# Optimization experiments

Measured on AMD Instinct MI355X. Metric: run time of the kernel, lower is better.

## Reference

```python
import jax, jax.numpy as jnp
import numpy as np


def _conv1x1(x, w, b):
    # x: (B, C, H, W), w: (O, C), b: (O,)  -> (B, O, H, W)
    return jnp.einsum('oc,bchw->bohw', w, x) + b[None, :, None, None]


def _branch(xq, xkv, wq, bq, wk, bk, wv, bv):
    B, C, H, W = xq.shape
    N = H * W
    q = _conv1x1(xq, wq, bq).reshape(B, -1, N)   # (B, d, N)
    k = _conv1x1(xkv, wk, bk).reshape(B, -1, N)  # (B, d, N)
    v = _conv1x1(xkv, wv, bv).reshape(B, C, N)   # (B, C, N)
    energy = jnp.einsum('bdi,bdj->bij', q, k)    # (B, N, N), no scale (as in source)
    attn = jax.nn.softmax(energy, axis=-1)
    out = jnp.einsum('bcj,bij->bci', v, attn)    # bmm(v, attn^T)
    return out.reshape(B, C, H, W)


def setup_inputs() -> dict:
    key = jax.random.key(0)
    ks = jax.random.split(key, 16)
    B, C, H, W = 4, 256, 64, 64
    d = C // 8
    s_in = 0.02
    inp = {
        'x1': jax.random.normal(ks[0], (B, C, H, W), jnp.float32),
        'x2': jax.random.normal(ks[1], (B, C, H, W), jnp.float32),
        'wq1': jax.random.normal(ks[2], (d, C), jnp.float32) * s_in,
        'bq1': jnp.zeros((d,), jnp.float32),
        'wk1': jax.random.normal(ks[3], (d, C), jnp.float32) * s_in,
        'bk1': jnp.zeros((d,), jnp.float32),
        'wv1': jax.random.normal(ks[4], (C, C), jnp.float32) * s_in,
        'bv1': jnp.zeros((C,), jnp.float32),
        'wq2': jax.random.normal(ks[5], (d, C), jnp.float32) * s_in,
        'bq2': jnp.zeros((d,), jnp.float32),
        'wk2': jax.random.normal(ks[6], (d, C), jnp.float32) * s_in,
        'bk2': jnp.zeros((d,), jnp.float32),
        'wv2': jax.random.normal(ks[7], (C, C), jnp.float32) * s_in,
        'bv2': jnp.zeros((C,), jnp.float32),
    }
    return inp


def reference(x1, x2, wq1, bq1, wk1, bk1, wv1, bv1, wq2, bq2, wk2, bk2, wv2, bv2):
    out1 = _branch(x1, x2, wq1, bq1, wk1, bk1, wv1, bv1)
    out2 = _branch(x1, x2, wq2, bq2, wk2, bk2, wv2, bv2)
    return x1 + x2 + out1 + out2
```

## Files before the change

kernel.cpp:

```cpp
#include <hip/hip_runtime.h>

#define N_TOK 4096
#define C_DIM 256
#define D_DIM 32

typedef float f32x4 __attribute__((ext_vector_type(4)));
typedef short short8 __attribute__((ext_vector_type(8)));
typedef unsigned short u16;

__device__ __forceinline__ u16 f2bf(float f) {
    unsigned int u = __builtin_bit_cast(unsigned int, f);
    u += 0x7fffu + ((u >> 16) & 1u);
    return (u16)(u >> 16);
}
__device__ __forceinline__ u16 f2bf_fast(float f) {
    return (u16)((__builtin_bit_cast(unsigned int, f) + 0x8000u) >> 16);
}
__device__ __forceinline__ float bf2f(u16 h) {
    unsigned int u = ((unsigned int)h) << 16;
    return __builtin_bit_cast(float, u);
}
__device__ __forceinline__ float exp2_fast(float x) {
#if __has_builtin(__builtin_amdgcn_exp2f)
    return __builtin_amdgcn_exp2f(x);
#else
    return exp2f(x);
#endif
}


__global__ __launch_bounds__(256) void qk_proj(
    const float* __restrict__ x1, const float* __restrict__ x2,
    const float* __restrict__ wq1, const float* __restrict__ bq1,
    const float* __restrict__ wk1, const float* __restrict__ bk1,
    const float* __restrict__ wq2, const float* __restrict__ bq2,
    const float* __restrict__ wk2, const float* __restrict__ bk2,
    u16* __restrict__ wsQ, u16* __restrict__ wsK)
{
    __shared__ float w_lds[32 * 256];
    const int ib = blockIdx.x;
    const int comb = blockIdx.y;
    const int b = comb & 3;
    const int branch = (comb >> 2) & 1;
    const int qk = comb >> 3;

    const float* x = qk ? x2 : x1;
    const float* w; const float* bias; u16* dst;
    if (qk == 0) { w = branch ? wq2 : wq1; bias = branch ? bq2 : bq1; dst = wsQ; }
    else         { w = branch ? wk2 : wk1; bias = branch ? bk2 : bk1; dst = wsK; }
    const int slice = branch * 4 + b;
    dst += (size_t)slice * N_TOK * D_DIM;
    const float osc = (qk == 0) ? 1.44269504088896341f : 1.0f;

    const int tid = threadIdx.x;
    for (int t = tid; t < 32 * 256; t += 256) w_lds[t] = w[t];
    __syncthreads();

    const int il = tid & 63;
    const int db = tid >> 6;
    const float* xc = x + (size_t)b * C_DIM * N_TOK + ib * 64 + il;

    float acc[8] = {0.f,0.f,0.f,0.f,0.f,0.f,0.f,0.f};
    for (int c4 = 0; c4 < 256; c4 += 4) {
        const float xv0 = xc[(size_t)(c4 + 0) * N_TOK];
        const float xv1 = xc[(size_t)(c4 + 1) * N_TOK];
        const float xv2 = xc[(size_t)(c4 + 2) * N_TOK];
        const float xv3 = xc[(size_t)(c4 + 3) * N_TOK];
#pragma unroll
        for (int mm = 0; mm < 8; ++mm) {
            const float4 wv = *(const float4*)&w_lds[(db * 8 + mm) * 256 + c4];
            acc[mm] += xv0 * wv.x + xv1 * wv.y + xv2 * wv.z + xv3 * wv.w;
        }
    }
    short8 pack;
#pragma unroll
    for (int mm = 0; mm < 8; ++mm)
        pack[mm] = (short)f2bf((acc[mm] + bias[db * 8 + mm]) * osc);
    *(short8*)(dst + (size_t)(ib * 64 + il) * D_DIM + db * 8) = pack;
}

__device__ __forceinline__ void stage_xt(u16* xtb, const float* xb, int ks,
                                         int wave, int lane)
{
    const int j  = (wave & 1) * 64 + lane;
    const int cb = (wave >> 1) * 16;
    const float* xp = xb + (size_t)(ks * 32 + cb) * N_TOK + j;
    u16 vals[16];
#pragma unroll
    for (int qq = 0; qq < 16; ++qq) vals[qq] = f2bf(xp[(size_t)qq * N_TOK]);
    const int swz = (j >> 1) & 3;
    u16* row = xtb + j * 32;
    const int c0 = cb >> 3;
    *(short8*)&row[((c0    ) ^ swz) * 8] = *(const short8*)&vals[0];
    *(short8*)&row[((c0 + 1) ^ swz) * 8] = *(const short8*)&vals[8];
}

__global__ __launch_bounds__(256, 2) void v_proj(
    const float* __restrict__ x2,
    const float* __restrict__ wv1, const float* __restrict__ bv1,
    const float* __restrict__ wv2, const float* __restrict__ bv2,
    u16* __restrict__ wsV)
{
    __shared__ __align__(16) u16 wl[128 * 256];
    __shared__ __align__(16) u16 xt[2][128 * 32];

    const int jt = blockIdx.x, ct = blockIdx.y, s = blockIdx.z;
    const int branch = s >> 2, b = s & 3;
    const float* w    = branch ? wv2 : wv1;
    const float* bias = branch ? bv2 : bv1;
    u16* dst = wsV + (size_t)s * C_DIM * N_TOK;
    const float* xb = x2 + (size_t)b * C_DIM * N_TOK + jt * 128;

    const int tid = threadIdx.x;
    const int wave = tid >> 6, lane = tid & 63;
    const int wr = wave >> 1, wc = wave & 1;
    const int g = lane >> 4, li = lane & 15;

    {
        const int c = tid >> 1;
        const int kh = (tid & 1) * 128;
        const float* wrow = w + (size_t)(ct * 128 + c) * C_DIM + kh;
        u16* lrow = wl + c * 256;
#pragma unroll
        for (int kk = 0; kk < 128; kk += 8) {
            const float4 a0 = *(const float4*)&wrow[kk];
            const float4 a1 = *(const float4*)&wrow[kk + 4];
            u16 tmp[8] = {f2bf(a0.x), f2bf(a0.y), f2bf(a0.z), f2bf(a0.w),
                          f2bf(a1.x), f2bf(a1.y), f2bf(a1.z), f2bf(a1.w)};
            const int kc = (kh + kk) >> 3;
            *(short8*)&lrow[(kc ^ (c & 7)) * 8] = *(const short8*)tmp;
        }
    }
    stage_xt(&xt[0][0], xb, 0, wave, lane);
    __syncthreads();

    f32x4 acc[4][4];
#pragma unroll
    for (int mf = 0; mf < 4; ++mf)
#pragma unroll
        for (int nf = 0; nf < 4; ++nf) acc[mf][nf] = (f32x4){0.f, 0.f, 0.f, 0.f};

    int buf = 0;
    for (int ks = 0; ks < 8; ++ks) {
        if (ks < 7) stage_xt(&xt[buf ^ 1][0], xb, ks + 1, wave, lane);

        short8 af[4], bf[4];
#pragma unroll
        for (int mf = 0; mf < 4; ++mf) {
            const int c = wr * 64 + mf * 16 + li;
            af[mf] = *(const short8*)&wl[c * 256 + (((ks * 4 + g) ^ (li & 7)) * 8)];
        }
#pragma unroll
        for (int nf = 0; nf < 4; ++nf) {
            const int j = wc * 64 + nf * 16 + li;
            bf[nf] = *(const short8*)&xt[buf][j * 32 + ((g ^ ((j >> 1) & 3)) * 8)];
        }
        __builtin_amdgcn_s_setprio(1);
#pragma unroll
        for (int mf = 0; mf < 4; ++mf)
#pragma unroll
            for (int nf = 0; nf < 4; ++nf)
                acc[mf][nf] = __builtin_amdgcn_mfma_f32_16x16x32_bf16(
                    af[mf], bf[nf], acc[mf][nf], 0, 0, 0);
        __builtin_amdgcn_s_setprio(0);
        __syncthreads();
        buf ^= 1;
    }

#pragma unroll
    for (int mf = 0; mf < 4; ++mf) {
#pragma unroll
        for (int r = 0; r < 4; ++r) {
            const int c = ct * 128 + wr * 64 + mf * 16 + 4 * g + r;
            const float bv = bias[c];
            const int cswz = (c >> 1) & 3;
            u16* crow = dst + c * 32;
#pragma unroll
            for (int nf = 0; nf < 4; ++nf) {
                const int j = jt * 128 + wc * 64 + nf * 16 + li;
                const int pos = ((j >> 3) & 3) ^ cswz;
                crow[(size_t)(j >> 5) * 8192 + pos * 8 + (j & 7)] =
                    f2bf(acc[mf][nf][r] + bv);
            }
        }
    }
}

__global__ __launch_bounds__(256, 4) void attn_fwd(
    const u16* __restrict__ Q, const u16* __restrict__ K,
    const u16* __restrict__ V, u16* __restrict__ O)
{
    __shared__ __align__(16) short vlds[2][2][128 * 32];
    __shared__ float lscr[2][2][64][2];

    const int n  = blockIdx.x;
    const int s  = n & 7;
    const int ib = (n >> 3) & 63;
    const int ct = n >> 9;
    const u16* q = Q + (size_t)s * N_TOK * D_DIM;
    const u16* k = K + (size_t)s * N_TOK * D_DIM;
    const u16* v = V + (size_t)s * C_DIM * N_TOK + ct * 4096;
    u16*       o = O + (size_t)s * N_TOK * C_DIM + ct * 128;

    const int tid  = threadIdx.x;
    const int wave = tid >> 6;
    const int lane = tid & 63;
    const int grp  = wave >> 1;
    const int wg   = wave & 1;
    const int g    = lane >> 4;
    const int li   = lane & 15;
    const int i0   = ib * 64 + wg * 32;
    const int jbase = grp * (N_TOK / 2);
    const int NP = N_TOK / 2 / 32;

    short8 qf[2];
    qf[0] = *(const short8*)(q + (size_t)(i0 + li) * D_DIM + 8 * g);
    qf[1] = *(const short8*)(q + (size_t)(i0 + 16 + li) * D_DIM + 8 * g);

    f32x4 acc[2][8];
#pragma unroll
    for (int it = 0; it < 2; ++it)
#pragma unroll
        for (int cf = 0; cf < 8; ++cf) acc[it][cf] = (f32x4){0.f, 0.f, 0.f, 0.f};
    float lsum[2] = {0.f, 0.f};

    const int roff = (g ^ ((li >> 1) & 3)) << 3;

    {
        const u16* tile = v + (size_t)(jbase >> 5) * 8192;
#pragma unroll
        for (int ii = 0; ii < 4; ++ii) {
            const int off = (wg * 4 + ii) * 512;
            __builtin_amdgcn_global_load_lds(
                (const __attribute__((address_space(1))) void*)(tile + off + lane * 8),
                (__attribute__((address_space(3))) void*)(&vlds[grp][0][0] + off),
                16, 0, 0);
        }
    }
    __syncthreads();

    int buf = 0;
    for (int p = 0; p < NP; ++p) {
        if (p < NP - 1) {
            const u16* tile = v + (size_t)((jbase + (p + 1) * 32) >> 5) * 8192;
            short* dst = &vlds[grp][buf ^ 1][0];
#pragma unroll
            for (int ii = 0; ii < 4; ++ii) {
                const int off = (wg * 4 + ii) * 512;
                __builtin_amdgcn_global_load_lds(
                    (const __attribute__((address_space(1))) void*)(tile + off + lane * 8),
                    (__attribute__((address_space(3))) void*)(dst + off),
                    16, 0, 0);
            }
        }

        const int j0 = jbase + p * 32;
        const short8 ke = *(const short8*)(k + (size_t)(j0 + 2 * li    ) * D_DIM + 8 * g);
        const short8 ko = *(const short8*)(k + (size_t)(j0 + 2 * li + 1) * D_DIM + 8 * g);

        const f32x4 z = (f32x4){0.f, 0.f, 0.f, 0.f};
        short8 pa[2];
#pragma unroll
        for (int it = 0; it < 2; ++it) {
            f32x4 se = __builtin_amdgcn_mfma_f32_16x16x32_bf16(ke, qf[it], z, 0, 0, 0);
            f32x4 so = __builtin_amdgcn_mfma_f32_16x16x32_bf16(ko, qf[it], z, 0, 0, 0);
            float pe[4], po[4];
#pragma unroll
            for (int r = 0; r < 4; ++r) {
                pe[r] = exp2_fast(se[r]);
                po[r] = exp2_fast(so[r]);
            }
            lsum[it] += ((pe[0] + po[0]) + (pe[1] + po[1]))
                      + ((pe[2] + po[2]) + (pe[3] + po[3]));
#pragma unroll
            for (int r = 0; r < 4; ++r) {
                pa[it][2 * r]     = (short)f2bf_fast(pe[r]);
                pa[it][2 * r + 1] = (short)f2bf_fast(po[r]);
            }
        }

        const short* vb = &vlds[grp][buf][0];
        __builtin_amdgcn_s_setprio(1);
#pragma unroll
        for (int cf = 0; cf < 8; ++cf) {
            const short8 vf = *(const short8*)&vb[(cf * 16 + li) * 32 + roff];
            acc[0][cf] = __builtin_amdgcn_mfma_f32_16x16x32_bf16(pa[0], vf, acc[0][cf], 0, 0, 0);
            acc[1][cf] = __builtin_amdgcn_mfma_f32_16x16x32_bf16(pa[1], vf, acc[1][cf], 0, 0, 0);
        }
        __builtin_amdgcn_s_setprio(0);
        __syncthreads();
        buf ^= 1;
    }

#pragma unroll
    for (int it = 0; it < 2; ++it) {
        lsum[it] += __shfl_xor(lsum[it], 16);
        lsum[it] += __shfl_xor(lsum[it], 32);
        lscr[grp][wg][lane][it] = lsum[it];
    }

    f32x4* pv = (f32x4*)&vlds[0][0][0];
#pragma unroll
    for (int it = 0; it < 2; ++it) {
        __syncthreads();
        if (grp == 1) {
#pragma unroll
            for (int cf = 0; cf < 8; ++cf)
                pv[(wg * 8 + cf) * 64 + lane] = acc[it][cf];
        }
        __syncthreads();
        if (grp == 0) {
#pragma unroll
            for (int cf = 0; cf < 8; ++cf) {
                const f32x4 o4 = pv[(wg * 8 + cf) * 64 + lane];
                acc[it][cf][0] += o4[0]; acc[it][cf][1] += o4[1];
                acc[it][cf][2] += o4[2]; acc[it][cf][3] += o4[3];
            }
        }
    }

    if (grp == 0) {
#pragma unroll
        for (int it = 0; it < 2; ++it) {
            const float linv = 1.0f / (lscr[0][wg][lane][it] + lscr[1][wg][lane][it]);
            float lr[4];
#pragma unroll
            for (int r = 0; r < 4; ++r) lr[r] = __shfl(linv, 4 * g + r);
#pragma unroll
            for (int cf = 0; cf < 8; ++cf)
#pragma unroll
                for (int r = 0; r < 4; ++r)
                    o[(size_t)(i0 + it * 16 + 4 * g + r) * C_DIM + cf * 16 + li] =
                        f2bf(acc[it][cf][r] * lr[r]);
        }
    }
}

__global__ __launch_bounds__(256) void epilogue(
    const float* __restrict__ x1, const float* __restrict__ x2,
    const u16* __restrict__ O, float* __restrict__ out)
{
    __shared__ float tl[64][65];
    const int it = blockIdx.x, ct = blockIdx.y, b = blockIdx.z;
    const int tid = threadIdx.x;
    const int cl = tid & 63, r0 = tid >> 6;

    const u16* O1 = O + (size_t)(b)     * N_TOK * C_DIM;
    const u16* O2 = O + (size_t)(4 + b) * N_TOK * C_DIM;

#pragma unroll
    for (int rr = 0; rr < 16; ++rr) {
        const int il = r0 + rr * 4;
        const size_t off = (size_t)(it * 64 + il) * C_DIM + ct * 64 + cl;
        tl[il][cl] = bf2f(O1[off]) + bf2f(O2[off]);
    }
    __syncthreads();
#pragma unroll
    for (int rr = 0; rr < 16; ++rr) {
        const int c2 = r0 + rr * 4;
        const size_t idx = ((size_t)b * C_DIM + ct * 64 + c2) * N_TOK + it * 64 + cl;
        out[idx] = x1[idx] + x2[idx] + tl[cl][c2];
    }
}

extern "C" void kernel_launch(void* const* d_in, const int* in_sizes, int n_in,
                              void* d_out, int out_size, void* d_ws, size_t ws_size,
                              hipStream_t stream)
{
    const float* x1  = (const float*)d_in[0];
    const float* x2  = (const float*)d_in[1];
    const float* wq1 = (const float*)d_in[2];
    const float* bq1 = (const float*)d_in[3];
    const float* wk1 = (const float*)d_in[4];
    const float* bk1 = (const float*)d_in[5];
    const float* wv1 = (const float*)d_in[6];
    const float* bv1 = (const float*)d_in[7];
    const float* wq2 = (const float*)d_in[8];
    const float* bq2 = (const float*)d_in[9];
    const float* wk2 = (const float*)d_in[10];
    const float* bk2 = (const float*)d_in[11];
    const float* wv2 = (const float*)d_in[12];
    const float* bv2 = (const float*)d_in[13];
    float* out = (float*)d_out;

    u16* wsQ = (u16*)d_ws;
    u16* wsK = wsQ + (size_t)8 * N_TOK * D_DIM;
    u16* wsV = wsK + (size_t)8 * N_TOK * D_DIM;
    u16* wsO = wsV + (size_t)8 * C_DIM * N_TOK;

    qk_proj<<<dim3(64, 16), 256, 0, stream>>>(x1, x2, wq1, bq1, wk1, bk1,
                                              wq2, bq2, wk2, bk2, wsQ, wsK);
    v_proj<<<dim3(32, 2, 8), 256, 0, stream>>>(x2, wv1, bv1, wv2, bv2, wsV);
    attn_fwd<<<dim3(1024), 256, 0, stream>>>(wsQ, wsK, wsV, wsO);
    epilogue<<<dim3(64, 4, 4), 256, 0, stream>>>(x1, x2, wsO, out);
}
```

Before: 161.8 us.

## Triple-buffer V tiles and prefetch K two iterations ahead in attention loop

```diff
diff --git a/kernel.cpp b/kernel.cpp
--- a/kernel.cpp
+++ b/kernel.cpp
@@ -186,11 +186,24 @@
     }
 }
 
+__device__ __forceinline__ void stage_v32c(const u16* vhalf, short* dst,
+                                           int wg, int lane, int j0)
+{
+    const u16* tile = vhalf + (size_t)(j0 >> 5) * 8192;
+#pragma unroll
+    for (int ii = 0; ii < 4; ++ii) {
+        const int off = (wg * 4 + ii) * 512;
+        __builtin_amdgcn_global_load_lds(
+            (const __attribute__((address_space(1))) void*)(tile + off + lane * 8),
+            (__attribute__((address_space(3))) void*)(dst + off), 16, 0, 0);
+    }
+}
+
 __global__ __launch_bounds__(256, 4) void attn_fwd(
     const u16* __restrict__ Q, const u16* __restrict__ K,
     const u16* __restrict__ V, u16* __restrict__ O)
 {
-    __shared__ __align__(16) short vlds[2][2][128 * 32];
+    __shared__ __align__(16) short vlds[2][3][128 * 32];
     __shared__ float lscr[2][2][64][2];
 
     const int n  = blockIdx.x;
@@ -226,44 +239,30 @@
 
     const int roff = (g ^ ((li >> 1) & 3)) << 3;
 
-    {
-        const u16* tile = v + (size_t)(jbase >> 5) * 8192;
-#pragma unroll
-        for (int ii = 0; ii < 4; ++ii) {
-            const int off = (wg * 4 + ii) * 512;
-            __builtin_amdgcn_global_load_lds(
-                (const __attribute__((address_space(1))) void*)(tile + off + lane * 8),
-                (__attribute__((address_space(3))) void*)(&vlds[grp][0][0] + off),
-                16, 0, 0);
-        }
-    }
-    __syncthreads();
-
-    int buf = 0;
+    stage_v32c(v, &vlds[grp][0][0], wg, lane, jbase);
+    short8 keC = *(const short8*)(k + (size_t)(jbase + 2 * li    ) * D_DIM + 8 * g);
+    short8 koC = *(const short8*)(k + (size_t)(jbase + 2 * li + 1) * D_DIM + 8 * g);
+    stage_v32c(v, &vlds[grp][1][0], wg, lane, jbase + 32);
+    short8 keN = *(const short8*)(k + (size_t)(jbase + 32 + 2 * li) * D_DIM + 8 * g);
+    short8 koN = *(const short8*)(k + (size_t)(jbase + 33 + 2 * li) * D_DIM + 8 * g);
+    asm volatile("s_waitcnt vmcnt(8)" ::: "memory");
+    __builtin_amdgcn_s_barrier();
+
+    int bcur = 0;
     for (int p = 0; p < NP; ++p) {
-        if (p < NP - 1) {
-            const u16* tile = v + (size_t)((jbase + (p + 1) * 32) >> 5) * 8192;
-            short* dst = &vlds[grp][buf ^ 1][0];
-#pragma unroll
-            for (int ii = 0; ii < 4; ++ii) {
-                const int off = (wg * 4 + ii) * 512;
-                __builtin_amdgcn_global_load_lds(
-                    (const __attribute__((address_space(1))) void*)(tile + off + lane * 8),
-                    (__attribute__((address_space(3))) void*)(dst + off),
-                    16, 0, 0);
-            }
-        }
-
-        const int j0 = jbase + p * 32;
-        const short8 ke = *(const short8*)(k + (size_t)(j0 + 2 * li    ) * D_DIM + 8 * g);
-        const short8 ko = *(const short8*)(k + (size_t)(j0 + 2 * li + 1) * D_DIM + 8 * g);
+        int t2 = p + 2; if (t2 >= NP) t2 -= NP;
+        const int j2 = jbase + t2 * 32;
+        int b2 = bcur + 2; if (b2 >= 3) b2 -= 3;
+        stage_v32c(v, &vlds[grp][b2][0], wg, lane, j2);
+        const short8 ket = *(const short8*)(k + (size_t)(j2 + 2 * li    ) * D_DIM + 8 * g);
+        const short8 kot = *(const short8*)(k + (size_t)(j2 + 2 * li + 1) * D_DIM + 8 * g);
 
         const f32x4 z = (f32x4){0.f, 0.f, 0.f, 0.f};
         short8 pa[2];
 #pragma unroll
         for (int it = 0; it < 2; ++it) {
-            f32x4 se = __builtin_amdgcn_mfma_f32_16x16x32_bf16(ke, qf[it], z, 0, 0, 0);
-            f32x4 so = __builtin_amdgcn_mfma_f32_16x16x32_bf16(ko, qf[it], z, 0, 0, 0);
+            f32x4 se = __builtin_amdgcn_mfma_f32_16x16x32_bf16(keC, qf[it], z, 0, 0, 0);
+            f32x4 so = __builtin_amdgcn_mfma_f32_16x16x32_bf16(koC, qf[it], z, 0, 0, 0);
             float pe[4], po[4];
 #pragma unroll
             for (int r = 0; r < 4; ++r) {
@@ -279,7 +278,7 @@
             }
         }
 
-        const short* vb = &vlds[grp][buf][0];
+        const short* vb = &vlds[grp][bcur][0];
         __builtin_amdgcn_s_setprio(1);
 #pragma unroll
         for (int cf = 0; cf < 8; ++cf) {
@@ -288,8 +287,12 @@
             acc[1][cf] = __builtin_amdgcn_mfma_f32_16x16x32_bf16(pa[1], vf, acc[1][cf], 0, 0, 0);
         }
         __builtin_amdgcn_s_setprio(0);
-        __syncthreads();
-        buf ^= 1;
+
+        asm volatile("s_waitcnt vmcnt(8)" ::: "memory");
+        __builtin_amdgcn_s_barrier();
+
+        keC = keN; koC = koN; keN = ket; koN = kot;
+        bcur = (bcur == 2) ? 0 : bcur + 1;
     }
 
 #pragma unroll
```

Measured after the change: 215.5 us. 33.2% more time.

## Store V and softmax probabilities in FP8 and use FP8 MFMA for PV

Applied to the files above, without the earlier changes.

```diff
diff --git a/kernel.cpp b/kernel.cpp
--- a/kernel.cpp
+++ b/kernel.cpp
@@ -1,4 +1,5 @@
 #include <hip/hip_runtime.h>
+#include <hip/hip_fp8.h>
 
 #define N_TOK 4096
 #define C_DIM 256
@@ -7,14 +8,13 @@
 typedef float f32x4 __attribute__((ext_vector_type(4)));
 typedef short short8 __attribute__((ext_vector_type(8)));
 typedef unsigned short u16;
+typedef unsigned char u8;
+typedef long long i64;
 
 __device__ __forceinline__ u16 f2bf(float f) {
     unsigned int u = __builtin_bit_cast(unsigned int, f);
     u += 0x7fffu + ((u >> 16) & 1u);
     return (u16)(u >> 16);
-}
-__device__ __forceinline__ u16 f2bf_fast(float f) {
-    return (u16)((__builtin_bit_cast(unsigned int, f) + 0x8000u) >> 16);
 }
 __device__ __forceinline__ float bf2f(u16 h) {
     unsigned int u = ((unsigned int)h) << 16;
@@ -26,6 +26,19 @@
 #else
     return exp2f(x);
 #endif
+}
+template<bool HI>
+__device__ __forceinline__ int pk_fp8(float a, float b, int old) {
+#if __has_builtin(__builtin_amdgcn_cvt_pk_fp8_f32)
+    return __builtin_amdgcn_cvt_pk_fp8_f32(a, b, old, HI);
+#else
+    __hip_fp8_e4m3 fa(a), fb(b);
+    int v = (int)fa.__x | ((int)fb.__x << 8);
+    return HI ? ((old & 0xffff) | (v << 16)) : ((old & ~0xffff) | (v & 0xffff));
+#endif
+}
+__device__ __forceinline__ u8 f2fp8(float f) {
+    return (u8)(pk_fp8<false>(f, f, 0) & 0xff);
 }
 
 
@@ -99,7 +112,7 @@
     const float* __restrict__ x2,
     const float* __restrict__ wv1, const float* __restrict__ bv1,
     const float* __restrict__ wv2, const float* __restrict__ bv2,
-    u16* __restrict__ wsV)
+    u8* __restrict__ wsV)
 {
     __shared__ __align__(16) u16 wl[128 * 256];
     __shared__ __align__(16) u16 xt[2][128 * 32];
@@ -108,7 +121,7 @@
     const int branch = s >> 2, b = s & 3;
     const float* w    = branch ? wv2 : wv1;
     const float* bias = branch ? bv2 : bv1;
-    u16* dst = wsV + (size_t)s * C_DIM * N_TOK;
+    u8* dstB = wsV + (size_t)s * N_TOK * C_DIM;
     const float* xb = x2 + (size_t)b * C_DIM * N_TOK + jt * 128;
 
     const int tid = threadIdx.x;
@@ -173,14 +186,11 @@
         for (int r = 0; r < 4; ++r) {
             const int c = ct * 128 + wr * 64 + mf * 16 + 4 * g + r;
             const float bv = bias[c];
-            const int cswz = (c >> 1) & 3;
-            u16* crow = dst + c * 32;
 #pragma unroll
             for (int nf = 0; nf < 4; ++nf) {
                 const int j = jt * 128 + wc * 64 + nf * 16 + li;
-                const int pos = ((j >> 3) & 3) ^ cswz;
-                crow[(size_t)(j >> 5) * 8192 + pos * 8 + (j & 7)] =
-                    f2bf(acc[mf][nf][r] + bv);
+                dstB[(size_t)(j >> 5) * 8192 + ((j >> 3) & 3) * 2048
+                     + c * 8 + (j & 7)] = f2fp8(acc[mf][nf][r] + bv);
             }
         }
     }
@@ -188,9 +198,9 @@
 
 __global__ __launch_bounds__(256, 4) void attn_fwd(
     const u16* __restrict__ Q, const u16* __restrict__ K,
-    const u16* __restrict__ V, u16* __restrict__ O)
-{
-    __shared__ __align__(16) short vlds[2][2][128 * 32];
+    const u8* __restrict__ V, u16* __restrict__ O)
+{
+    __shared__ __align__(16) u8 vlds[2][2][4096];
     __shared__ float lscr[2][2][64][2];
 
     const int n  = blockIdx.x;
@@ -199,7 +209,7 @@
     const int ct = n >> 9;
     const u16* q = Q + (size_t)s * N_TOK * D_DIM;
     const u16* k = K + (size_t)s * N_TOK * D_DIM;
-    const u16* v = V + (size_t)s * C_DIM * N_TOK + ct * 4096;
+    const u8*  v = V + (size_t)s * N_TOK * C_DIM + ct * 1024;
     u16*       o = O + (size_t)s * N_TOK * C_DIM + ct * 128;
 
     const int tid  = threadIdx.x;
@@ -224,16 +234,14 @@
         for (int cf = 0; cf < 8; ++cf) acc[it][cf] = (f32x4){0.f, 0.f, 0.f, 0.f};
     float lsum[2] = {0.f, 0.f};
 
-    const int roff = (g ^ ((li >> 1) & 3)) << 3;
-
     {
-        const u16* tile = v + (size_t)(jbase >> 5) * 8192;
-#pragma unroll
-        for (int ii = 0; ii < 4; ++ii) {
-            const int off = (wg * 4 + ii) * 512;
+        const u8* tile = v + (size_t)(jbase >> 5) * 8192;
+#pragma unroll
+        for (int ii = 0; ii < 2; ++ii) {
+            const int p = wg * 2 + ii;
             __builtin_amdgcn_global_load_lds(
-                (const __attribute__((address_space(1))) void*)(tile + off + lane * 8),
-                (__attribute__((address_space(3))) void*)(&vlds[grp][0][0] + off),
+                (const __attribute__((address_space(1))) void*)(tile + p * 2048 + lane * 16),
+                (__attribute__((address_space(3))) void*)(&vlds[grp][0][0] + p * 1024),
                 16, 0, 0);
         }
     }
@@ -242,14 +250,14 @@
     int buf = 0;
     for (int p = 0; p < NP; ++p) {
         if (p < NP - 1) {
-            const u16* tile = v + (size_t)((jbase + (p + 1) * 32) >> 5) * 8192;
-            short* dst = &vlds[grp][buf ^ 1][0];
-#pragma unroll
-            for (int ii = 0; ii < 4; ++ii) {
-                const int off = (wg * 4 + ii) * 512;
+            const u8* tile = v + (size_t)((jbase + (p + 1) * 32) >> 5) * 8192;
+            u8* dst = &vlds[grp][buf ^ 1][0];
+#pragma unroll
+            for (int ii = 0; ii < 2; ++ii) {
+                const int pc = wg * 2 + ii;
                 __builtin_amdgcn_global_load_lds(
-                    (const __attribute__((address_space(1))) void*)(tile + off + lane * 8),
-                    (__attribute__((address_space(3))) void*)(dst + off),
+                    (const __attribute__((address_space(1))) void*)(tile + pc * 2048 + lane * 16),
+                    (__attribute__((address_space(3))) void*)(dst + pc * 1024),
                     16, 0, 0);
             }
         }
@@ -259,7 +267,7 @@
         const short8 ko = *(const short8*)(k + (size_t)(j0 + 2 * li + 1) * D_DIM + 8 * g);
 
         const f32x4 z = (f32x4){0.f, 0.f, 0.f, 0.f};
-        short8 pa[2];
+        i64 paL[2];
 #pragma unroll
         for (int it = 0; it < 2; ++it) {
             f32x4 se = __builtin_amdgcn_mfma_f32_16x16x32_bf16(ke, qf[it], z, 0, 0, 0);
@@ -272,20 +280,21 @@
             }
             lsum[it] += ((pe[0] + po[0]) + (pe[1] + po[1]))
                       + ((pe[2] + po[2]) + (pe[3] + po[3]));
-#pragma unroll
-            for (int r = 0; r < 4; ++r) {
-                pa[it][2 * r]     = (short)f2bf_fast(pe[r]);
-                pa[it][2 * r + 1] = (short)f2bf_fast(po[r]);
-            }
-        }
-
-        const short* vb = &vlds[grp][buf][0];
+            int w0 = pk_fp8<false>(pe[0], po[0], 0);
+            w0     = pk_fp8<true >(pe[1], po[1], w0);
+            int w1 = pk_fp8<false>(pe[2], po[2], 0);
+            w1     = pk_fp8<true >(pe[3], po[3], w1);
+            paL[it] = (i64)(((unsigned long long)(unsigned)w1 << 32) | (unsigned)w0);
+        }
+
+        const u8* vb = &vlds[grp][buf][0];
+        const i64* vbL = (const i64*)(vb + g * 1024 + li * 8);
         __builtin_amdgcn_s_setprio(1);
 #pragma unroll
         for (int cf = 0; cf < 8; ++cf) {
-            const short8 vf = *(const short8*)&vb[(cf * 16 + li) * 32 + roff];
-            acc[0][cf] = __builtin_amdgcn_mfma_f32_16x16x32_bf16(pa[0], vf, acc[0][cf], 0, 0, 0);
-            acc[1][cf] = __builtin_amdgcn_mfma_f32_16x16x32_bf16(pa[1], vf, acc[1][cf], 0, 0, 0);
+            const i64 vfL = vbL[cf * 16];
+            acc[0][cf] = __builtin_amdgcn_mfma_f32_16x16x32_fp8_fp8(paL[0], vfL, acc[0][cf], 0, 0, 0);
+            acc[1][cf] = __builtin_amdgcn_mfma_f32_16x16x32_fp8_fp8(paL[1], vfL, acc[1][cf], 0, 0, 0);
         }
         __builtin_amdgcn_s_setprio(0);
         __syncthreads();
@@ -385,8 +394,8 @@
 
     u16* wsQ = (u16*)d_ws;
     u16* wsK = wsQ + (size_t)8 * N_TOK * D_DIM;
-    u16* wsV = wsK + (size_t)8 * N_TOK * D_DIM;
-    u16* wsO = wsV + (size_t)8 * C_DIM * N_TOK;
+    u8*  wsV = (u8*)(wsK + (size_t)8 * N_TOK * D_DIM);
+    u16* wsO = (u16*)(wsV + (size_t)8 * N_TOK * C_DIM);
 
     qk_proj<<<dim3(64, 16), 256, 0, stream>>>(x1, x2, wq1, bq1, wk1, bk1,
                                               wq2, bq2, wk2, bk2, wsQ, wsK);
```

Result: faster. 139.4 us (median of 2 runs) (-13.8%).
